# Performance work log

Measured on AMD Instinct MI355X. Metric: run time of the kernel, lower is better.

The kernel has to match this reference:

```python
import jax, jax.numpy as jnp
import numpy as np

B, S, D, E, H, K = 2, 2048, 1024, 8, 2048, 2
EM_ITERS = 5
LB_WEIGHT = 0.1
EPS = 1e-8


def setup_inputs() -> dict:
    key = jax.random.key(0)
    ks = jax.random.split(key, 12)
    sc = 0.02
    return {
        "x": jax.random.normal(ks[0], (B, S, D), jnp.float32),
        "gate_W": jax.random.normal(ks[1], (D, E), jnp.float32) * sc,
        "gate_b": jnp.zeros((E,), jnp.float32),
        "gate_temp": jnp.ones((1,), jnp.float32),
        "W1": jax.random.normal(ks[2], (E, D, H), jnp.float32) * sc,
        "b1": jnp.zeros((E, H), jnp.float32),
        "W2": jax.random.normal(ks[3], (E, H, D), jnp.float32) * sc,
        "b2": jnp.zeros((E, D), jnp.float32),
        "sW1": jax.random.normal(ks[4], (D, H), jnp.float32) * sc,
        "sb1": jnp.zeros((H,), jnp.float32),
        "sW2": jax.random.normal(ks[5], (H, D), jnp.float32) * sc,
        "sb2": jnp.zeros((D,), jnp.float32),
    }


def reference(x, gate_W, gate_b, gate_temp, W1, b1, W2, b2, sW1, sb1, sW2, sb2):
    Bq, Sq, Dq = x.shape
    T = Bq * Sq
    xf = x.reshape(T, Dq)  # (T, D)

    # Router: gate linear + learned temperature
    gate_logits = xf @ gate_W + gate_b              # (T, E)
    tempered = gate_logits / gate_temp               # (T, E)
    expert_weights = jax.nn.softmax(tempered, axis=-1)
    _, topk_idx = jax.lax.top_k(expert_weights, K)   # (T, K) int32
    first = topk_idx[:, 0]

    # Load-balance loss: KL(uniform || empirical top-1 usage) (fresh counters)
    usage = jnp.zeros((E,), jnp.float32).at[first].add(1.0)
    actual = usage / jnp.float32(T)
    actual = actual + EPS
    actual = actual / actual.sum()
    u = jnp.float32(1.0 / E)
    kl = jnp.sum(u * (jnp.log(u) - jnp.log(actual)))
    load_balance_loss = LB_WEIGHT * kl

    # EM expert-load reweighting on tempered logits
    scores = jax.nn.softmax(tempered, axis=-1)       # (T, E)
    p = jnp.full((E,), 1.0 / E, jnp.float32)
    for _ in range(EM_ITERS):
        ea = scores * p                               # (T, E)
        ea = ea / (ea.sum(axis=-1, keepdims=True) + EPS)
        counts = ea.sum(axis=0)                       # (E,)
        p = counts / (counts.sum() + EPS)
    balanced = scores * p                             # (T, E)

    # All-expert FFN (dense, equivalent to per-expert masked compute)
    h = jax.nn.relu(jnp.einsum('td,edh->teh', xf, W1) + b1)  # (T, E, H)
    eo = jnp.einsum('teh,ehd->ted', h, W2) + b2              # (T, E, D)

    # Combine top-k experts with balanced weights
    w_k = jnp.take_along_axis(balanced, topk_idx, axis=1)        # (T, K)
    out_k = jnp.take_along_axis(eo, topk_idx[:, :, None], axis=1)  # (T, K, D)
    out = jnp.einsum('tk,tkd->td', w_k, out_k)                   # (T, D)

    # Shared expert, weighted by 0.1
    shared = jax.nn.relu(xf @ sW1 + sb1) @ sW2 + sb2
    out = out + 0.1 * shared

    return out.reshape(Bq, Sq, Dq), load_balance_loss
```

## Files before the change

kernel.cpp:

```cpp
#include <hip/hip_runtime.h>
#include <math.h>

#define T_TOK 4096
#define D_DIM 1024
#define H_DIM 2048
#define NE 8
#define EPSF 1e-8f
#define G1_GEMM 448
#define G2_GEMM 224
#define NTR128 1152

typedef __attribute__((ext_vector_type(8))) short bf16x8;
typedef __attribute__((ext_vector_type(4))) float f32x4;

__device__ __forceinline__ unsigned short f2bf(float f) {
  unsigned u = __float_as_uint(f);
  u += 0x7fffu + ((u >> 16) & 1u);
  return (unsigned short)(u >> 16);
}

__device__ __forceinline__ void gload_lds16(const void* g, void* l) {
  __builtin_amdgcn_global_load_lds(
      (const __attribute__((address_space(1))) unsigned int*)g,
      (__attribute__((address_space(3))) unsigned int*)l, 16, 0, 0);
}

#define WAITV(n) asm volatile("s_waitcnt vmcnt(" #n ")" ::: "memory")
#define BARR()                                  \
  do {                                          \
    asm volatile("" ::: "memory");              \
    __builtin_amdgcn_s_barrier();               \
    asm volatile("" ::: "memory");              \
  } while (0)

__device__ __forceinline__ void transpose_tile128(const float* __restrict__ src,
                                                  unsigned short* __restrict__ dst,
                                                  int R, int C, int r0, int c0, int tid,
                                                  float* tile) {
#pragma unroll
  for (int k = 0; k < 8; ++k) {
    int id = tid + k * 512;
    int row = id >> 5, c4 = (id & 31) * 4;
    float4 v = *(const float4*)(src + (size_t)(r0 + row) * C + c0 + c4);
    float* tr = tile + row * 129 + c4;
    tr[0] = v.x; tr[1] = v.y; tr[2] = v.z; tr[3] = v.w;
  }
  __syncthreads();
#pragma unroll
  for (int k = 0; k < 4; ++k) {
    int id = tid + k * 512;
    int oc = id >> 4;
    int rbase = (id & 15) * 8;
    uint4 wv;
    unsigned* wp = (unsigned*)&wv;
#pragma unroll
    for (int j = 0; j < 4; ++j) {
      unsigned lo = f2bf(tile[(rbase + 2 * j) * 129 + oc]);
      unsigned hi = f2bf(tile[(rbase + 2 * j + 1) * 129 + oc]);
      wp[j] = lo | (hi << 16);
    }
    *(uint4*)(dst + (size_t)(c0 + oc) * R + r0 + rbase) = wv;
  }
}

__global__ __launch_bounds__(512, 4) void gate_kernel(
    const float* __restrict__ x, const float* __restrict__ gW, const float* __restrict__ gb,
    const float* __restrict__ gtemp, unsigned short* __restrict__ xb,
    float* __restrict__ scores, int* __restrict__ idx,
    unsigned* __restrict__ usage, unsigned* __restrict__ cnt, int* __restrict__ perm) {
  __shared__ float gWl[D_DIM * 9];
  __shared__ int toks[16];
  int tid = threadIdx.x, wave = tid >> 6, lane = tid & 63;
  int t0 = blockIdx.x * 8;

#pragma unroll
  for (int k = 0; k < 4; ++k) {
    int q = tid + k * 512;
    float4 f = ((const float4*)gW)[q];
    int d = q >> 1, eo = (q & 1) * 4;
    float* dst = &gWl[d * 9 + eo];
    dst[0] = f.x; dst[1] = f.y; dst[2] = f.z; dst[3] = f.w;
  }
  __syncthreads();

  int t = t0 + wave;
  const float* xr = x + (size_t)t * D_DIM;
  unsigned short* xbr = xb + (size_t)t * D_DIM;
  float part[NE];
#pragma unroll
  for (int e = 0; e < NE; ++e) part[e] = 0.f;
#pragma unroll
  for (int i = 0; i < 16; ++i) {
    int d = lane + 64 * i;
    float xv = xr[d];
    xbr[d] = f2bf(xv);
    const float* g = &gWl[d * 9];
#pragma unroll
    for (int e = 0; e < NE; ++e) part[e] += xv * g[e];
  }
#pragma unroll
  for (int e = 0; e < NE; ++e) {
    float v = part[e];
    for (int off = 32; off; off >>= 1) v += __shfl_xor(v, off);
    part[e] = v;
  }
  float temp = gtemp[0];
  float mx = -1e30f;
#pragma unroll
  for (int e = 0; e < NE; ++e) { part[e] = (part[e] + gb[e]) / temp; mx = fmaxf(mx, part[e]); }
  float s = 0.f;
#pragma unroll
  for (int e = 0; e < NE; ++e) { part[e] = expf(part[e] - mx); s += part[e]; }
  float inv = 1.0f / s;
#pragma unroll
  for (int e = 0; e < NE; ++e) part[e] *= inv;
  if (lane == 0) {
    float4* sp = (float4*)(scores + (size_t)t * NE);
    sp[0] = make_float4(part[0], part[1], part[2], part[3]);
    sp[1] = make_float4(part[4], part[5], part[6], part[7]);
    int i0 = 0; float b0 = part[0];
#pragma unroll
    for (int e = 1; e < NE; ++e) if (part[e] > b0) { b0 = part[e]; i0 = e; }
    int i1 = -1; float b1 = -1e30f;
#pragma unroll
    for (int e = 0; e < NE; ++e) if (e != i0 && part[e] > b1) { b1 = part[e]; i1 = e; }
    idx[t * 2] = i0; idx[t * 2 + 1] = i1;
    toks[wave * 2] = i0; toks[wave * 2 + 1] = i1;
  }
  __syncthreads();
  if (tid < NE) {
    int c0 = 0, c1 = 0;
#pragma unroll
    for (int j = 0; j < 8; ++j) {
      if (toks[j * 2] == tid) ++c0;
      if (toks[j * 2 + 1] == tid) ++c1;
    }
    if (c0) atomicAdd(&usage[tid], (unsigned)c0);
    int tot = c0 + c1;
    if (tot) {
      unsigned b = atomicAdd(&cnt[tid], (unsigned)tot);
      int p = 0;
#pragma unroll
      for (int j = 0; j < 8; ++j) {
        if (toks[j * 2] == tid) perm[(size_t)tid * T_TOK + b + p++] = (t0 + j) * 2;
        if (toks[j * 2 + 1] == tid) perm[(size_t)tid * T_TOK + b + p++] = (t0 + j) * 2 + 1;
      }
    }
  }
}

__global__ __launch_bounds__(512) void transW1_kernel(
    const float* __restrict__ W1, const float* __restrict__ sW1,
    unsigned short* __restrict__ W1t, unsigned short* __restrict__ sW1t) {
  __shared__ float tile[128 * 129];
  int l = blockIdx.x;
  int m = l >> 7, rem = l & 127;
  int c0 = (rem & 15) * 128, r0 = (rem >> 4) * 128;
  const float* src = (m < NE) ? W1 + (size_t)m * D_DIM * H_DIM : sW1;
  unsigned short* dst = (m < NE) ? W1t + (size_t)m * D_DIM * H_DIM : sW1t;
  transpose_tile128(src, dst, D_DIM, H_DIM, r0, c0, threadIdx.x, tile);
}

__device__ __forceinline__ void em_block512(const float* __restrict__ scores,
                                            const unsigned* __restrict__ usage,
                                            float* __restrict__ p_out, float* __restrict__ loss_out,
                                            int tid, char* smem) {
  float* p_sh = (float*)smem;
  float* cw = p_sh + 8;
  float* counts_sh = cw + 64;
  int wave = tid >> 6, lane = tid & 63;
  float s[8][NE];
#pragma unroll
  for (int rr = 0; rr < 8; ++rr) {
    int row = tid + rr * 512;
    const float4* sp = (const float4*)(scores + (size_t)row * NE);
    float4 a = sp[0], b = sp[1];
    s[rr][0] = a.x; s[rr][1] = a.y; s[rr][2] = a.z; s[rr][3] = a.w;
    s[rr][4] = b.x; s[rr][5] = b.y; s[rr][6] = b.z; s[rr][7] = b.w;
  }
  if (tid < NE) p_sh[tid] = 1.0f / NE;
  __syncthreads();
  for (int it = 0; it < 5; ++it) {
    float p[NE];
#pragma unroll
    for (int e = 0; e < NE; ++e) p[e] = p_sh[e];
    float c[NE];
#pragma unroll
    for (int e = 0; e < NE; ++e) c[e] = 0.f;
#pragma unroll
    for (int rr = 0; rr < 8; ++rr) {
      float denom = 0.f;
#pragma unroll
      for (int e = 0; e < NE; ++e) denom += s[rr][e] * p[e];
      float inv = 1.0f / (denom + EPSF);
#pragma unroll
      for (int e = 0; e < NE; ++e) c[e] += s[rr][e] * p[e] * inv;
    }
#pragma unroll
    for (int e = 0; e < NE; ++e) {
      float v = c[e];
      for (int off = 32; off; off >>= 1) v += __shfl_xor(v, off);
      c[e] = v;
    }
    if (lane == 0) {
#pragma unroll
      for (int e = 0; e < NE; ++e) cw[wave * 8 + e] = c[e];
    }
    __syncthreads();
    if (tid < NE) {
      float tot = 0.f;
#pragma unroll
      for (int w = 0; w < 8; ++w) tot += cw[w * 8 + tid];
      counts_sh[tid] = tot;
    }
    __syncthreads();
    if (tid < NE) {
      float total = 0.f;
#pragma unroll
      for (int e = 0; e < NE; ++e) total += counts_sh[e];
      p_sh[tid] = counts_sh[tid] / (total + EPSF);
    }
    __syncthreads();
  }
  if (tid < NE) p_out[tid] = p_sh[tid];
  if (tid == 0) {
    float actual[NE]; float norm = 0.f;
#pragma unroll
    for (int e = 0; e < NE; ++e) { actual[e] = (float)usage[e] / (float)T_TOK + EPSF; norm += actual[e]; }
    float u = 1.0f / NE;
    float kl = 0.f;
#pragma unroll
    for (int e = 0; e < NE; ++e) kl += u * (logf(u) - logf(actual[e] / norm));
    loss_out[0] = 0.1f * kl;
  }
}

template <int KDIM, int NDIM, bool RELU, bool MODE1>
__device__ __forceinline__ void gemm_body(
    unsigned short* lds, int flat,
    const unsigned short* __restrict__ A, const unsigned short* __restrict__ WE,
    const unsigned short* __restrict__ WS, const float* __restrict__ biasE,
    const float* __restrict__ biasS, const int* __restrict__ perm,
    const unsigned* __restrict__ cnt, void* __restrict__ outp) {
  constexpr int BM = 256, BN = 256, BK = 64;
  constexpr int NT = NDIM / BN;
  constexpr int NKT = KDIM / BK;

  int tc[9];
#pragma unroll
  for (int i = 0; i < NE; ++i) tc[i] = ((int)cnt[i] + 255) >> 8;
  tc[8] = T_TOK / 256;
  int nt = 0;
#pragma unroll
  for (int i = 0; i < 9; ++i) nt += tc[i];
  int W = nt * NT;
  int xcd = flat & 7, pos = flat >> 3;
  int q = W >> 3, r = W & 7;
  int mycount = q + (xcd < r ? 1 : 0);
  if (pos >= mycount) return;
  int mystart = xcd * q + (xcd < r ? xcd : r);
  int w = mystart + pos;
  int ti = w / NT;
  int n0 = (w % NT) * BN;
  int e = 0, mt = ti;
  while (mt >= tc[e]) { mt -= tc[e]; ++e; }
  int m0 = mt * BM;
  int cnt_e = (e == NE) ? T_TOK : (int)cnt[e];

  const unsigned short* Bmat = (e == NE) ? WS : WE + (size_t)e * KDIM * NDIM;
  const float* bias = (e == NE) ? biasS : biasE + (size_t)e * NDIM;

  int tid = threadIdx.x, wave = tid >> 6, lane = tid & 63;
  int wm = wave >> 1, wn = wave & 1;
  int frow = lane & 15, fks = lane >> 4;

  int srow = wave * 8 + (lane >> 3);
  int sslot = lane & 7;
  const unsigned short* aptr[2][2];
  const unsigned short* bptr[2][2];
#pragma unroll
  for (int h = 0; h < 2; ++h)
#pragma unroll
    for (int j = 0; j < 2; ++j) {
      int rr = h * 128 + j * 64 + srow;
      int colsw = (sslot ^ (rr & 7)) << 3;
      int ar = m0 + rr;
      if (ar > cnt_e - 1) ar = cnt_e - 1;
      int gar;
      if (e == NE) gar = MODE1 ? ar : (2 * T_TOK + ar);
      else { int v = perm[(size_t)e * T_TOK + ar]; gar = MODE1 ? (v >> 1) : v; }
      aptr[h][j] = A + (size_t)gar * KDIM + colsw;
      bptr[h][j] = Bmat + (size_t)(n0 + rr) * KDIM + colsw;
    }

  auto stA = [&](int t, int h) {
    int dbe = (t & 1) * 16384;
    int k0 = t * BK;
    gload_lds16(aptr[h][0] + k0, &lds[dbe + h * 8192 + wave * 512]);
    gload_lds16(aptr[h][1] + k0, &lds[dbe + h * 8192 + wave * 512 + 4096]);
  };
  auto stB = [&](int t, int h) {
    int dbe = (t & 1) * 16384;
    int k0 = t * BK;
    gload_lds16(bptr[h][0] + k0, &lds[32768 + dbe + h * 8192 + wave * 512]);
    gload_lds16(bptr[h][1] + k0, &lds[32768 + dbe + h * 8192 + wave * 512 + 4096]);
  };

  auto rdA = [&](int dbe, int ks, int m) -> bf16x8 {
    int rr = wm * 64 + m * 16 + frow;
    int slot = (ks * 4 + fks) ^ (rr & 7);
    return *(const bf16x8*)&lds[dbe + rr * 64 + slot * 8];
  };
  auto rdB = [&](int dbe, int ks, int bh, int jj) -> bf16x8 {
    int rr = bh * 128 + jj * 32 + wn * 16 + frow;
    int slot = (ks * 4 + fks) ^ (rr & 7);
    return *(const bf16x8*)&lds[32768 + dbe + rr * 64 + slot * 8];
  };

  f32x4 acc[4][8];
#pragma unroll
  for (int m = 0; m < 4; ++m)
#pragma unroll
    for (int nn = 0; nn < 8; ++nn) acc[m][nn] = (f32x4){0.f, 0.f, 0.f, 0.f};

  stA(0, 0); stA(0, 1);
  stB(0, 0); stB(0, 1);
  stA(1, 0); stA(1, 1);
  WAITV(6);
  BARR();

  for (int t = 0; t < NKT; ++t) {
    const int dbe = (t & 1) * 16384;
    bf16x8 a0[4], a1[4], bfr[4];

#pragma unroll
    for (int m = 0; m < 4; ++m) a0[m] = rdA(dbe, 0, m);
#pragma unroll
    for (int jj = 0; jj < 4; ++jj) bfr[jj] = rdB(dbe, 0, 0, jj);
    if (t + 1 < NKT) stB(t + 1, 0);
    BARR();
    __builtin_amdgcn_s_setprio(1);
#pragma unroll
    for (int m = 0; m < 4; ++m)
#pragma unroll
      for (int jj = 0; jj < 4; ++jj)
        acc[m][jj] = __builtin_amdgcn_mfma_f32_16x16x32_bf16(a0[m], bfr[jj], acc[m][jj], 0, 0, 0);
    __builtin_amdgcn_s_setprio(0);
    BARR();

#pragma unroll
    for (int m = 0; m < 4; ++m) a1[m] = rdA(dbe, 1, m);
#pragma unroll
    for (int jj = 0; jj < 4; ++jj) bfr[jj] = rdB(dbe, 1, 0, jj);
    if (t + 1 < NKT) stB(t + 1, 1);
    BARR();
    __builtin_amdgcn_s_setprio(1);
#pragma unroll
    for (int m = 0; m < 4; ++m)
#pragma unroll
      for (int jj = 0; jj < 4; ++jj)
        acc[m][jj] = __builtin_amdgcn_mfma_f32_16x16x32_bf16(a1[m], bfr[jj], acc[m][jj], 0, 0, 0);
    __builtin_amdgcn_s_setprio(0);
    if (t + 1 < NKT) { WAITV(8); } else { WAITV(0); }
    BARR();

#pragma unroll
    for (int jj = 0; jj < 4; ++jj) bfr[jj] = rdB(dbe, 0, 1, jj);
    if (t + 2 < NKT) stA(t + 2, 0);
    BARR();
    __builtin_amdgcn_s_setprio(1);
#pragma unroll
    for (int m = 0; m < 4; ++m)
#pragma unroll
      for (int jj = 0; jj < 4; ++jj)
        acc[m][4 + jj] = __builtin_amdgcn_mfma_f32_16x16x32_bf16(a0[m], bfr[jj], acc[m][4 + jj], 0, 0, 0);
    __builtin_amdgcn_s_setprio(0);
    BARR();

#pragma unroll
    for (int jj = 0; jj < 4; ++jj) bfr[jj] = rdB(dbe, 1, 1, jj);
    if (t + 2 < NKT) stA(t + 2, 1);
    BARR();
    __builtin_amdgcn_s_setprio(1);
#pragma unroll
    for (int m = 0; m < 4; ++m)
#pragma unroll
      for (int jj = 0; jj < 4; ++jj)
        acc[m][4 + jj] = __builtin_amdgcn_mfma_f32_16x16x32_bf16(a1[m], bfr[jj], acc[m][4 + jj], 0, 0, 0);
    __builtin_amdgcn_s_setprio(0);
    if (t + 1 < NKT) {
      if (t + 2 < NKT) { WAITV(6); } else { WAITV(2); }
    }
    BARR();
  }

#pragma unroll
  for (int m = 0; m < 4; ++m) {
#pragma unroll
    for (int qq = 0; qq < 4; ++qq) {
      int rt = wm * 64 + m * 16 + (lane >> 4) * 4 + qq;
      if (m0 + rt >= cnt_e) continue;
      int rr;
      if (e == NE) rr = 2 * T_TOK + m0 + rt;
      else rr = perm[(size_t)e * T_TOK + m0 + rt];
#pragma unroll
      for (int nn = 0; nn < 8; ++nn) {
        int col = n0 + (nn >> 2) * 128 + (nn & 3) * 32 + wn * 16 + (lane & 15);
        float val = acc[m][nn][qq] + bias[col];
        if (RELU) val = fmaxf(val, 0.f);
        if (MODE1)
          ((unsigned short*)outp)[(size_t)rr * NDIM + col] = f2bf(val);
        else
          ((float*)outp)[(size_t)rr * NDIM + col] = val;
      }
    }
  }
}

__global__ __launch_bounds__(512, 2) void gemm1_kernel(
    const unsigned short* __restrict__ xb, const unsigned short* __restrict__ W1t,
    const unsigned short* __restrict__ sW1t, const float* __restrict__ b1,
    const float* __restrict__ sb1, const int* __restrict__ perm, const unsigned* __restrict__ cnt,
    unsigned short* __restrict__ Hbuf,
    const float* __restrict__ W2, const float* __restrict__ sW2,
    unsigned short* __restrict__ W2t, unsigned short* __restrict__ sW2t,
    const float* __restrict__ scores, const unsigned* __restrict__ usage,
    float* __restrict__ pbuf, float* __restrict__ loss_out) {
  __shared__ char smem[131072];
  int flat = blockIdx.x;
  if (flat < G1_GEMM) {
    gemm_body<D_DIM, H_DIM, true, true>((unsigned short*)smem, flat, xb, W1t, sW1t, b1, sb1,
                                        perm, cnt, (void*)Hbuf);
    return;
  }
  int l = flat - G1_GEMM;
  if (l < NTR128) {
    int m = l >> 7, rem = l & 127;
    int c0 = (rem & 7) * 128, r0 = (rem >> 3) * 128;
    const float* src = (m < NE) ? W2 + (size_t)m * H_DIM * D_DIM : sW2;
    unsigned short* dst = (m < NE) ? W2t + (size_t)m * H_DIM * D_DIM : sW2t;
    transpose_tile128(src, dst, H_DIM, D_DIM, r0, c0, threadIdx.x, (float*)smem);
    return;
  }
  em_block512(scores, usage, pbuf, loss_out, threadIdx.x, smem);
}

template <int KDIM, int NDIM, bool RELU, bool MODE1>
__global__ __launch_bounds__(512, 2) void gemm_kernel(
    const unsigned short* __restrict__ A, const unsigned short* __restrict__ WE,
    const unsigned short* __restrict__ WS, const float* __restrict__ biasE,
    const float* __restrict__ biasS, const int* __restrict__ perm,
    const unsigned* __restrict__ cnt, void* __restrict__ outp) {
  __shared__ char smem[131072];
  gemm_body<KDIM, NDIM, RELU, MODE1>((unsigned short*)smem, blockIdx.x, A, WE, WS, biasE, biasS,
                                     perm, cnt, outp);
}

__global__ void combine_kernel(const float* __restrict__ ebuf, const float* __restrict__ scores,
                               const float* __restrict__ p, const int* __restrict__ idx,
                               float* __restrict__ out) {
  int gid = blockIdx.x * blockDim.x + threadIdx.x;
  int t = gid >> 8;
  int d4 = gid & 255;
  int e0 = idx[t * 2], e1 = idx[t * 2 + 1];
  float w0 = scores[(size_t)t * NE + e0] * p[e0];
  float w1 = scores[(size_t)t * NE + e1] * p[e1];
  const float4* r0 = (const float4*)(ebuf + (size_t)(t * 2) * D_DIM);
  const float4* r1 = (const float4*)(ebuf + (size_t)(t * 2 + 1) * D_DIM);
  const float4* rs = (const float4*)(ebuf + (size_t)(2 * T_TOK + t) * D_DIM);
  float4 a = r0[d4], b = r1[d4], c = rs[d4];
  float4 o;
  o.x = w0 * a.x + w1 * b.x + 0.1f * c.x;
  o.y = w0 * a.y + w1 * b.y + 0.1f * c.y;
  o.z = w0 * a.z + w1 * b.z + 0.1f * c.z;
  o.w = w0 * a.w + w1 * b.w + 0.1f * c.w;
  ((float4*)out)[gid] = o;
}

extern "C" void kernel_launch(void* const* d_in, const int* in_sizes, int n_in,
                              void* d_out, int out_size, void* d_ws, size_t ws_size,
                              hipStream_t stream) {
  const float* x     = (const float*)d_in[0];
  const float* gW    = (const float*)d_in[1];
  const float* gb    = (const float*)d_in[2];
  const float* gtemp = (const float*)d_in[3];
  const float* W1    = (const float*)d_in[4];
  const float* b1    = (const float*)d_in[5];
  const float* W2    = (const float*)d_in[6];
  const float* b2    = (const float*)d_in[7];
  const float* sW1   = (const float*)d_in[8];
  const float* sb1   = (const float*)d_in[9];
  const float* sW2   = (const float*)d_in[10];
  const float* sb2   = (const float*)d_in[11];
  float* out = (float*)d_out;

  char* ws = (char*)d_ws;
  size_t off = 0;
  auto take = [&](size_t b) { char* ptr = ws + off; off += (b + 255) & ~(size_t)255; return ptr; };
  unsigned short* xb   = (unsigned short*)take((size_t)T_TOK * D_DIM * 2);
  unsigned short* W1t  = (unsigned short*)take((size_t)NE * H_DIM * D_DIM * 2);
  unsigned short* sW1t = (unsigned short*)take((size_t)H_DIM * D_DIM * 2);
  unsigned short* W2t  = (unsigned short*)take((size_t)NE * D_DIM * H_DIM * 2);
  unsigned short* sW2t = (unsigned short*)take((size_t)D_DIM * H_DIM * 2);
  unsigned short* Hbuf = (unsigned short*)take((size_t)3 * T_TOK * H_DIM * 2);
  float* ebuf          = (float*)take((size_t)3 * T_TOK * D_DIM * 4);
  float* scores        = (float*)take((size_t)T_TOK * NE * 4);
  int* idx             = (int*)take((size_t)T_TOK * 2 * 4);
  int* perm            = (int*)take((size_t)NE * T_TOK * 4);
  unsigned* cnt        = (unsigned*)take(256);
  unsigned* usage      = (unsigned*)take(256);
  float* pbuf          = (float*)take(256);
  (void)n_in; (void)in_sizes; (void)out_size; (void)ws_size;

  hipMemsetAsync(cnt, 0, 512, stream);
  gate_kernel<<<512, 512, 0, stream>>>(x, gW, gb, gtemp, xb, scores, idx, usage, cnt, perm);
  transW1_kernel<<<NTR128, 512, 0, stream>>>(W1, sW1, W1t, sW1t);
  gemm1_kernel<<<G1_GEMM + NTR128 + 1, 512, 0, stream>>>(
      xb, W1t, sW1t, b1, sb1, perm, cnt, Hbuf, W2, sW2, W2t, sW2t, scores, usage, pbuf,
      out + (size_t)T_TOK * D_DIM);
  gemm_kernel<H_DIM, D_DIM, false, false><<<G2_GEMM, 512, 0, stream>>>(
      Hbuf, W2t, sW2t, b2, sb2, perm, cnt, (void*)ebuf);
  combine_kernel<<<(T_TOK * D_DIM / 4) / 256, 256, 0, stream>>>(ebuf, scores, pbuf, idx, out);
}
```

Measured before the change: 198.0 us.

## Merge gate and W1 transpose kernels; restructure GEMM main loop into two phases

The gate/routing kernel and the W1/sW1 transpose-to-bf16 kernel are fused into one launch, with block index selecting the role and a shared LDS buffer sized for the larger user. This removes one kernel launch and lets both independent jobs run concurrently. Separately, the GEMM inner loop is collapsed from four barrier-separated MFMA phases to two: both K sub-slices of A and B fragments are read at once, and prefetches are issued in pairs, with adjusted vmcnt waits. This halves barriers per K-step at the cost of more live fragment registers, which could reduce occupancy.

```diff
diff --git a/kernel.cpp b/kernel.cpp
--- a/kernel.cpp
+++ b/kernel.cpp
@@ -63,26 +63,36 @@
   }
 }
 
-__global__ __launch_bounds__(512, 4) void gate_kernel(
+__global__ __launch_bounds__(512, 4) void prep2_kernel(
     const float* __restrict__ x, const float* __restrict__ gW, const float* __restrict__ gb,
-    const float* __restrict__ gtemp, unsigned short* __restrict__ xb,
-    float* __restrict__ scores, int* __restrict__ idx,
+    const float* __restrict__ gtemp, const float* __restrict__ W1, const float* __restrict__ sW1,
+    unsigned short* __restrict__ W1t, unsigned short* __restrict__ sW1t,
+    unsigned short* __restrict__ xb, float* __restrict__ scores, int* __restrict__ idx,
     unsigned* __restrict__ usage, unsigned* __restrict__ cnt, int* __restrict__ perm) {
-  __shared__ float gWl[D_DIM * 9];
-  __shared__ int toks[16];
-  int tid = threadIdx.x, wave = tid >> 6, lane = tid & 63;
-  int t0 = blockIdx.x * 8;
-
+  __shared__ char psm[67584];
+  int b = blockIdx.x, tid = threadIdx.x;
+  if (b >= 512) {
+    int l = b - 512;
+    int m = l >> 7, rem = l & 127;
+    int c0 = (rem & 15) * 128, r0 = (rem >> 4) * 128;
+    const float* src = (m < NE) ? W1 + (size_t)m * D_DIM * H_DIM : sW1;
+    unsigned short* dst = (m < NE) ? W1t + (size_t)m * D_DIM * H_DIM : sW1t;
+    transpose_tile128(src, dst, D_DIM, H_DIM, r0, c0, tid, (float*)psm);
+    return;
+  }
+  float* gWl = (float*)psm;
+  int* toks = (int*)(psm + 36864);
+  int wave = tid >> 6, lane = tid & 63;
+  int t0 = b * 8;
 #pragma unroll
   for (int k = 0; k < 4; ++k) {
     int q = tid + k * 512;
     float4 f = ((const float4*)gW)[q];
     int d = q >> 1, eo = (q & 1) * 4;
-    float* dst = &gWl[d * 9 + eo];
-    dst[0] = f.x; dst[1] = f.y; dst[2] = f.z; dst[3] = f.w;
+    float* dstv = &gWl[d * 9 + eo];
+    dstv[0] = f.x; dstv[1] = f.y; dstv[2] = f.z; dstv[3] = f.w;
   }
   __syncthreads();
-
   int t = t0 + wave;
   const float* xr = x + (size_t)t * D_DIM;
   unsigned short* xbr = xb + (size_t)t * D_DIM;
@@ -138,27 +148,15 @@
     if (c0) atomicAdd(&usage[tid], (unsigned)c0);
     int tot = c0 + c1;
     if (tot) {
-      unsigned b = atomicAdd(&cnt[tid], (unsigned)tot);
+      unsigned bb = atomicAdd(&cnt[tid], (unsigned)tot);
       int p = 0;
 #pragma unroll
       for (int j = 0; j < 8; ++j) {
-        if (toks[j * 2] == tid) perm[(size_t)tid * T_TOK + b + p++] = (t0 + j) * 2;
-        if (toks[j * 2 + 1] == tid) perm[(size_t)tid * T_TOK + b + p++] = (t0 + j) * 2 + 1;
+        if (toks[j * 2] == tid) perm[(size_t)tid * T_TOK + bb + p++] = (t0 + j) * 2;
+        if (toks[j * 2 + 1] == tid) perm[(size_t)tid * T_TOK + bb + p++] = (t0 + j) * 2 + 1;
       }
     }
   }
-}
-
-__global__ __launch_bounds__(512) void transW1_kernel(
-    const float* __restrict__ W1, const float* __restrict__ sW1,
-    unsigned short* __restrict__ W1t, unsigned short* __restrict__ sW1t) {
-  __shared__ float tile[128 * 129];
-  int l = blockIdx.x;
-  int m = l >> 7, rem = l & 127;
-  int c0 = (rem & 15) * 128, r0 = (rem >> 4) * 128;
-  const float* src = (m < NE) ? W1 + (size_t)m * D_DIM * H_DIM : sW1;
-  unsigned short* dst = (m < NE) ? W1t + (size_t)m * D_DIM * H_DIM : sW1t;
-  transpose_tile128(src, dst, D_DIM, H_DIM, r0, c0, threadIdx.x, tile);
 }
 
 __device__ __forceinline__ void em_block512(const float* __restrict__ scores,
@@ -326,71 +324,57 @@
   stA(0, 0); stA(0, 1);
   stB(0, 0); stB(0, 1);
   stA(1, 0); stA(1, 1);
-  WAITV(6);
+  WAITV(4);
   BARR();
 
   for (int t = 0; t < NKT; ++t) {
     const int dbe = (t & 1) * 16384;
-    bf16x8 a0[4], a1[4], bfr[4];
+    bf16x8 a0[4], a1[4], b0[4], b1[4];
 
 #pragma unroll
     for (int m = 0; m < 4; ++m) a0[m] = rdA(dbe, 0, m);
 #pragma unroll
-    for (int jj = 0; jj < 4; ++jj) bfr[jj] = rdB(dbe, 0, 0, jj);
-    if (t + 1 < NKT) stB(t + 1, 0);
+    for (int m = 0; m < 4; ++m) a1[m] = rdA(dbe, 1, m);
+#pragma unroll
+    for (int jj = 0; jj < 4; ++jj) b0[jj] = rdB(dbe, 0, 0, jj);
+#pragma unroll
+    for (int jj = 0; jj < 4; ++jj) b1[jj] = rdB(dbe, 1, 0, jj);
+    if (t + 1 < NKT) { stB(t + 1, 0); stB(t + 1, 1); }
     BARR();
     __builtin_amdgcn_s_setprio(1);
 #pragma unroll
     for (int m = 0; m < 4; ++m)
 #pragma unroll
       for (int jj = 0; jj < 4; ++jj)
-        acc[m][jj] = __builtin_amdgcn_mfma_f32_16x16x32_bf16(a0[m], bfr[jj], acc[m][jj], 0, 0, 0);
+        acc[m][jj] = __builtin_amdgcn_mfma_f32_16x16x32_bf16(a0[m], b0[jj], acc[m][jj], 0, 0, 0);
+#pragma unroll
+    for (int m = 0; m < 4; ++m)
+#pragma unroll
+      for (int jj = 0; jj < 4; ++jj)
+        acc[m][jj] = __builtin_amdgcn_mfma_f32_16x16x32_bf16(a1[m], b1[jj], acc[m][jj], 0, 0, 0);
     __builtin_amdgcn_s_setprio(0);
     BARR();
 
 #pragma unroll
-    for (int m = 0; m < 4; ++m) a1[m] = rdA(dbe, 1, m);
-#pragma unroll
-    for (int jj = 0; jj < 4; ++jj) bfr[jj] = rdB(dbe, 1, 0, jj);
-    if (t + 1 < NKT) stB(t + 1, 1);
+    for (int jj = 0; jj < 4; ++jj) b0[jj] = rdB(dbe, 0, 1, jj);
+#pragma unroll
+    for (int jj = 0; jj < 4; ++jj) b1[jj] = rdB(dbe, 1, 1, jj);
+    if (t + 2 < NKT) { stA(t + 2, 0); stA(t + 2, 1); }
     BARR();
     __builtin_amdgcn_s_setprio(1);
 #pragma unroll
     for (int m = 0; m < 4; ++m)
 #pragma unroll
       for (int jj = 0; jj < 4; ++jj)
-        acc[m][jj] = __builtin_amdgcn_mfma_f32_16x16x32_bf16(a1[m], bfr[jj], acc[m][jj], 0, 0, 0);
+        acc[m][4 + jj] = __builtin_amdgcn_mfma_f32_16x16x32_bf16(a0[m], b0[jj], acc[m][4 + jj], 0, 0, 0);
+#pragma unroll
+    for (int m = 0; m < 4; ++m)
+#pragma unroll
+      for (int jj = 0; jj < 4; ++jj)
+        acc[m][4 + jj] = __builtin_amdgcn_mfma_f32_16x16x32_bf16(a1[m], b1[jj], acc[m][4 + jj], 0, 0, 0);
     __builtin_amdgcn_s_setprio(0);
-    if (t + 1 < NKT) { WAITV(8); } else { WAITV(0); }
-    BARR();
-
-#pragma unroll
-    for (int jj = 0; jj < 4; ++jj) bfr[jj] = rdB(dbe, 0, 1, jj);
-    if (t + 2 < NKT) stA(t + 2, 0);
-    BARR();
-    __builtin_amdgcn_s_setprio(1);
-#pragma unroll
-    for (int m = 0; m < 4; ++m)
-#pragma unroll
-      for (int jj = 0; jj < 4; ++jj)
-        acc[m][4 + jj] = __builtin_amdgcn_mfma_f32_16x16x32_bf16(a0[m], bfr[jj], acc[m][4 + jj], 0, 0, 0);
-    __builtin_amdgcn_s_setprio(0);
-    BARR();
-
-#pragma unroll
-    for (int jj = 0; jj < 4; ++jj) bfr[jj] = rdB(dbe, 1, 1, jj);
-    if (t + 2 < NKT) stA(t + 2, 1);
-    BARR();
-    __builtin_amdgcn_s_setprio(1);
-#pragma unroll
-    for (int m = 0; m < 4; ++m)
-#pragma unroll
-      for (int jj = 0; jj < 4; ++jj)
-        acc[m][4 + jj] = __builtin_amdgcn_mfma_f32_16x16x32_bf16(a1[m], bfr[jj], acc[m][4 + jj], 0, 0, 0);
-    __builtin_amdgcn_s_setprio(0);
-    if (t + 1 < NKT) {
-      if (t + 2 < NKT) { WAITV(6); } else { WAITV(2); }
-    }
+    if (t + 2 < NKT) { WAITV(4); }
+    else if (t + 1 < NKT) { WAITV(0); }
     BARR();
   }
 
@@ -513,8 +497,8 @@
   (void)n_in; (void)in_sizes; (void)out_size; (void)ws_size;
 
   hipMemsetAsync(cnt, 0, 512, stream);
-  gate_kernel<<<512, 512, 0, stream>>>(x, gW, gb, gtemp, xb, scores, idx, usage, cnt, perm);
-  transW1_kernel<<<NTR128, 512, 0, stream>>>(W1, sW1, W1t, sW1t);
+  prep2_kernel<<<512 + NTR128, 512, 0, stream>>>(x, gW, gb, gtemp, W1, sW1, W1t, sW1t, xb,
+                                                 scores, idx, usage, cnt, perm);
   gemm1_kernel<<<G1_GEMM + NTR128 + 1, 512, 0, stream>>>(
       xb, W1t, sW1t, b1, sb1, perm, cnt, Hbuf, W2, sW2, W2t, sW2t, scores, usage, pbuf,
       out + (size_t)T_TOK * D_DIM);
```

Result: no change. 196.3 us (-0.9%).
